# Kernel tuning notes

Hardware: AMD Instinct MI355X
Metric: run time of the kernel (lower is better)

Reference implementation:

```python
import jax, jax.numpy as jnp
import numpy as np

B, S, H, L = 4, 8192, 1024, 4
RATIOS = [1.0, 0.5, 0.25, 0.125]
H4 = H // 4


def _xavier(key, shape):
    fan_in, fan_out = shape[-2], shape[-1]
    std = np.sqrt(2.0 / (fan_in + fan_out)).astype(np.float32)
    return jax.random.normal(key, shape, dtype=jnp.float32) * std


def setup_inputs() -> dict:
    key = jax.random.key(0)
    ks = jax.random.split(key, 32)
    it = iter(ks)
    inp = {
        "keys": jax.random.normal(next(it), (B, S, H), dtype=jnp.float32),
        "values": jax.random.normal(next(it), (B, S, H), dtype=jnp.float32),
        # level predictors (same shape across levels -> stacked). Weights stored as [in, out].
        "Pw1": _xavier(next(it), (L, H, H4)),
        "Pb1": jnp.zeros((L, H4), dtype=jnp.float32),
        "Pw2": _xavier(next(it), (L, H4, 1)),
        "Pb2": jnp.zeros((L, 1), dtype=jnp.float32),
    }
    for l, r in enumerate(RATIOS):
        d = int(H * r)
        inp[f"cw1_{l}"] = _xavier(next(it), (H, d))
        inp[f"cb1_{l}"] = jnp.zeros((d,), dtype=jnp.float32)
        inp[f"cw2_{l}"] = _xavier(next(it), (d, H))
        inp[f"cb2_{l}"] = jnp.zeros((H,), dtype=jnp.float32)
    return inp


def reference(keys, values, Pw1, Pb1, Pw2, Pb2,
              cw1_0, cb1_0, cw2_0, cb2_0,
              cw1_1, cb1_1, cw2_1, cb2_1,
              cw1_2, cb1_2, cw2_2, cb2_2,
              cw1_3, cb1_3, cw2_3, cb2_3):
    comps = [
        (cw1_0, cb1_0, cw2_0, cb2_0),
        (cw1_1, cb1_1, cw2_1, cb2_1),
        (cw1_2, cb1_2, cw2_2, cb2_2),
        (cw1_3, cb1_3, cw2_3, cb2_3),
    ]

    def assign_levels(x):
        # per-level predictor: sigmoid(relu(x W1 + b1) W2 + b2) -> argmax over levels
        h = jax.nn.relu(jnp.einsum('bsh,lhd->lbsd', x, Pw1) + Pb1[:, None, None, :])
        p = jax.nn.sigmoid(jnp.einsum('lbsd,ldo->lbso', h, Pw2) + Pb2[:, None, None, :])
        return jnp.argmax(p[..., 0], axis=0)  # [B, S] int, first-max tiebreak like torch.argmax

    def compress(x, lev):
        out = jnp.zeros_like(x)
        for l, (w1, b1, w2, b2) in enumerate(comps):
            y = jax.nn.relu(x @ w1 + b1) @ w2 + b2  # bottleneck MLP for level l
            out = jnp.where((lev == l)[..., None], y, out)
        return out

    key_levels = assign_levels(keys)
    value_levels = assign_levels(values)
    return compress(keys, key_levels), compress(values, value_levels)
```

## Files before the change

### kernel.cpp

```cpp
#include <hip/hip_runtime.h>

#define NTOK 32768
#define MARGIN 0.08f

typedef __attribute__((ext_vector_type(8))) short bshort8;
typedef __attribute__((ext_vector_type(8))) unsigned short ushort8v;
typedef __attribute__((ext_vector_type(4))) float f32x4;

__device__ __forceinline__ unsigned short f2bf(float f) {
  unsigned u = __float_as_uint(f);
  u += 0x7fffu + ((u >> 16) & 1u);
  return (unsigned short)(u >> 16);
}
__device__ __forceinline__ float bf2f(unsigned short h) {
  return __uint_as_float((unsigned)h << 16);
}

__device__ __forceinline__ void gload16(const void* g, void* l) {
  __builtin_amdgcn_global_load_lds(
      (const __attribute__((address_space(1))) void*)g,
      (__attribute__((address_space(3))) void*)l, 16, 0, 0);
}

__global__ __launch_bounds__(256) void xconv_kernel(
    const float* __restrict__ keys, const float* __restrict__ vals,
    unsigned short* __restrict__ xbf) {
  const size_t stride = (size_t)gridDim.x * 256;
  const size_t half = (size_t)NTOK * 128;
  for (size_t u = (size_t)blockIdx.x * 256 + threadIdx.x;
       u < (size_t)2 * NTOK * 128; u += stride) {
    const float* s = (u < half) ? (keys + u * 8) : (vals + (u - half) * 8);
    float4 a = *(const float4*)s;
    float4 b = *(const float4*)(s + 4);
    ushort8v o;
    o[0] = f2bf(a.x); o[1] = f2bf(a.y); o[2] = f2bf(a.z); o[3] = f2bf(a.w);
    o[4] = f2bf(b.x); o[5] = f2bf(b.y); o[6] = f2bf(b.z); o[7] = f2bf(b.w);
    *(ushort8v*)(xbf + u * 8) = o;
  }
}

struct TrArgs {
  const float* src[12];
  unsigned short* dst[12];
  int R[12];
  int C[12];
};

__global__ __launch_bounds__(256) void convert_kernel(TrArgs ta) {
  __shared__ float t[32][33];
  const int mid = blockIdx.z;
  const int R = ta.R[mid], C = ta.C[mid];
  const int r0 = blockIdx.y * 32, c0 = blockIdx.x * 32;
  if (r0 >= R || c0 >= C) return;
  const float* __restrict__ src = ta.src[mid];
  unsigned short* __restrict__ dst = ta.dst[mid];
  const int tid = threadIdx.x;
#pragma unroll
  for (int it = 0; it < 4; ++it) {
    int r = it * 8 + (tid >> 5), c = tid & 31;
    t[r][c] = src[(size_t)(r0 + r) * C + c0 + c];
  }
  __syncthreads();
#pragma unroll
  for (int it = 0; it < 4; ++it) {
    int cc = it * 8 + (tid >> 5), rr = tid & 31;
    dst[(size_t)(c0 + cc) * R + r0 + rr] = f2bf(t[rr][cc]);
  }
}

#define M_PRED 0
#define M_L1   1
#define M_L2   2

struct GArgs {
  const unsigned short* xbf;
  const unsigned short* predW1T;
  const float* Pb1; const float* Pw2;
  float* logits;
  const unsigned short* cw1T[4];
  const unsigned short* cw2T[4];
  const float* cb1[4]; const float* cb2[4];
  unsigned short* h;
  const int* counts; const int* bins;
  const long long* hOff;
  float* out;
};

template<int MODE>
__global__ __launch_bounds__(256) void gemm_core(GArgs ga) {
  const int tid  = threadIdx.x;
  const int lane = tid & 63;
  const int wave = tid >> 6;

  int lev, tens, tile, n0;
  if constexpr (MODE == M_PRED) {
    const int combo = blockIdx.x;
    n0   = (combo & 1) * 128;
    lev  = (combo >> 1) & 3;
    tens = combo >> 3;
    tile = blockIdx.z;
  } else {
    n0   = blockIdx.x * 128;
    const int zz = blockIdx.y;
    lev  = zz & 3;
    tens = zz >> 2;
    tile = blockIdx.z;
  }
  const int z = tens * 4 + lev;
  const int d = 1024 >> lev;

  int cnt, K;
  const unsigned short* Bt;
  if constexpr (MODE == M_PRED) {
    cnt = NTOK; K = 1024;
    Bt = ga.predW1T + ((size_t)lev * 256 + n0) * 1024;
  } else if constexpr (MODE == M_L1) {
    cnt = ga.counts[z]; K = 1024;
    if (n0 >= d) return;
    Bt = ga.cw1T[lev] + (size_t)n0 * 1024;
  } else {
    cnt = ga.counts[z]; K = d;
    Bt = ga.cw2T[lev] + (size_t)n0 * (size_t)d;
  }
  if (tile * 128 >= cnt) return;
  const int nt = min(128, cnt - tile * 128);

  __shared__ __align__(16) char smem[33280];
  int* tokS = (int*)(smem + 32768);

  long long hoff = 0;
  if constexpr (MODE != M_PRED) hoff = ga.hOff[z];

  const int arow  = tid & 127;
  const int celem = (tid >> 7) * 8;
  const unsigned short* aP;
  if constexpr (MODE == M_PRED) {
    aP = ga.xbf + ((size_t)tens * NTOK + tile * 128 + arow) * 1024;
  } else if constexpr (MODE == M_L1) {
    int idx = tile * 128 + arow;
    if (idx >= cnt) idx = cnt - 1;
    aP = ga.xbf + ((size_t)tens * NTOK + ga.bins[(size_t)z * NTOK + idx]) * 1024;
  } else {
    int rg = tile * 128 + arow;
    if (rg >= cnt) rg = cnt - 1;
    aP = ga.h + hoff + (size_t)rg * d;
  }
  aP += celem;
  const unsigned short* bP = Bt + (size_t)arow * K + celem;

  if constexpr (MODE == M_L2) {
    if (tid < 128) {
      int idx = tile * 128 + tid;
      if (idx >= cnt) idx = cnt - 1;
      tokS[tid] = ga.bins[(size_t)z * NTOK + idx];
    }
  }

  f32x4 acc[4][4];
#pragma unroll
  for (int i = 0; i < 4; ++i)
#pragma unroll
    for (int j = 0; j < 4; ++j) acc[i][j] = (f32x4)0.f;

  const int wm = (wave & 1) * 64, wn = (wave >> 1) * 64;

  char* const As0 = smem + tid * 16;
  char* const As1 = As0 + 4096;
  char* const Bs0 = As0 + 16384;
  char* const Bs1 = As0 + 20480;

  gload16(aP,      As0); gload16(aP + 16, As1);
  gload16(bP,      Bs0); gload16(bP + 16, Bs1);
  aP += 32; bP += 32;
  __syncthreads();

  const int fro = (lane >> 4) * 2048 + (lane & 15) * 16;
  int bufo = 0;
  const int nk = K >> 5;
  for (int it = 0; it < nk; ++it) {
    if (it + 1 < nk) {
      const int bo = bufo ^ 8192;
      gload16(aP,      As0 + bo); gload16(aP + 16, As1 + bo);
      gload16(bP,      Bs0 + bo); gload16(bP + 16, Bs1 + bo);
      aP += 32; bP += 32;
    }
    const char* Ab = smem + bufo + fro;
    bshort8 af[4], bfr[4];
#pragma unroll
    for (int i = 0; i < 4; ++i)
      af[i] = *(const bshort8*)(Ab + (wm + i * 16) * 16);
#pragma unroll
    for (int j = 0; j < 4; ++j)
      bfr[j] = *(const bshort8*)(Ab + 16384 + (wn + j * 16) * 16);
#pragma unroll
    for (int i = 0; i < 4; ++i)
#pragma unroll
      for (int j = 0; j < 4; ++j)
        acc[i][j] = __builtin_amdgcn_mfma_f32_16x16x32_bf16(af[i], bfr[j], acc[i][j], 0, 0, 0);
    __syncthreads();
    bufo ^= 8192;
  }

  if constexpr (MODE == M_PRED) {
    const float* b1 = ga.Pb1 + lev * 256 + n0;
    const float* w2 = ga.Pw2 + lev * 256 + n0;
    float part[4][4];
#pragma unroll
    for (int i = 0; i < 4; ++i)
#pragma unroll
      for (int r = 0; r < 4; ++r) part[i][r] = 0.f;
#pragma unroll
    for (int j = 0; j < 4; ++j) {
      int col = wn + j * 16 + (lane & 15);
      float bb = b1[col], ww = w2[col];
#pragma unroll
      for (int i = 0; i < 4; ++i)
#pragma unroll
        for (int r = 0; r < 4; ++r)
          part[i][r] = fmaf(fmaxf(acc[i][j][r] + bb, 0.f), ww, part[i][r]);
    }
#pragma unroll
    for (int m = 1; m < 16; m <<= 1)
#pragma unroll
      for (int i = 0; i < 4; ++i)
#pragma unroll
        for (int r = 0; r < 4; ++r)
          part[i][r] += __shfl_xor(part[i][r], m, 64);
    if ((lane & 15) == 0) {
      float* lg = ga.logits + (size_t)z * NTOK;
#pragma unroll
      for (int i = 0; i < 4; ++i)
#pragma unroll
        for (int r = 0; r < 4; ++r) {
          int row = tile * 128 + wm + i * 16 + (lane >> 4) * 4 + r;
          atomicAdd(&lg[row], part[i][r]);
        }
    }
  } else if constexpr (MODE == M_L1) {
    const float* b1 = ga.cb1[lev];
    unsigned short* Hs = (unsigned short*)smem;
#pragma unroll
    for (int i = 0; i < 4; ++i)
#pragma unroll
      for (int j = 0; j < 4; ++j) {
        int col = wn + j * 16 + (lane & 15);
        float bb = b1[n0 + col];
#pragma unroll
        for (int r = 0; r < 4; ++r) {
          int row = wm + i * 16 + (lane >> 4) * 4 + r;
          Hs[row * 128 + col] = f2bf(fmaxf(acc[i][j][r] + bb, 0.f));
        }
      }
    __syncthreads();
    unsigned short* hout = ga.h + hoff;
#pragma unroll
    for (int p = 0; p < 8; ++p) {
      int idx = p * 256 + tid;
      int row = idx >> 4;
      int cc  = (idx & 15) * 8;
      int rg = tile * 128 + row;
      if (rg < cnt)
        *(uint4*)(hout + (size_t)rg * d + n0 + cc) = *(const uint4*)(Hs + row * 128 + cc);
    }
  } else {
    const float* b2 = ga.cb2[lev];
    float* outT = ga.out + (size_t)tens * NTOK * 1024;
#pragma unroll
    for (int i = 0; i < 4; ++i)
#pragma unroll
      for (int r = 0; r < 4; ++r) {
        int row = wm + i * 16 + (lane >> 4) * 4 + r;
        if (row < nt) {
          int tok = tokS[row];
#pragma unroll
          for (int j = 0; j < 4; ++j) {
            int col = n0 + wn + j * 16 + (lane & 15);
            outT[(size_t)tok * 1024 + col] = acc[i][j][r] + b2[col];
          }
        }
      }
  }
}

__global__ __launch_bounds__(256) void argmax_margin_kernel(
    const float* __restrict__ logits, const float* __restrict__ Pb2,
    int* __restrict__ counts, int* __restrict__ bins,
    int* __restrict__ rcnt, int* __restrict__ rlist) {
  int i = blockIdx.x * 256 + threadIdx.x;
  if (i >= 2 * NTOK) return;
  int tens = i >> 15;
  int tok  = i & (NTOK - 1);
  const float* lg = logits + (size_t)tens * 4 * NTOK;
  float best = lg[tok] + Pb2[0];
  int bl = 0;
  float sec = -3.4e38f;
#pragma unroll
  for (int l = 1; l < 4; ++l) {
    float v = lg[(size_t)l * NTOK + tok] + Pb2[l];
    if (v > best) { sec = best; best = v; bl = l; }
    else if (v > sec) sec = v;
  }
  if (best - sec < MARGIN) {
    int pos = atomicAdd(&rcnt[tens], 1);
    rlist[tens * NTOK + pos] = tok;
  } else {
    int bin = tens * 4 + bl;
    int pos = atomicAdd(&counts[bin], 1);
    bins[(size_t)bin * NTOK + pos] = tok;
  }
}

__global__ __launch_bounds__(256) void recheck_gemm(
    const float* __restrict__ keys, const float* __restrict__ vals,
    const float* __restrict__ Pw1, const float* __restrict__ Pb1,
    const float* __restrict__ Pw2, const float* __restrict__ Pb2,
    const int* __restrict__ rcnt, const int* __restrict__ rlist,
    float* __restrict__ logitsR) {
  const int tid  = threadIdx.x;
  const int lev  = blockIdx.y;
  const int tens = blockIdx.z;
  const int cnt  = rcnt[tens];
  const float* __restrict__ X = tens ? vals : keys;
  const float* __restrict__ W = Pw1 + (size_t)lev * 1024 * 256;

  __shared__ float Xs[32][68];
  __shared__ float Ws[32][256];
  __shared__ float red[64][33];
  __shared__ int tokS[64];

  const int tokg = tid >> 5;
  const int colg = tid & 31;

  for (int tile = blockIdx.x; tile * 64 < cnt; tile += gridDim.x) {
    __syncthreads();
    if (tid < 64) {
      int s = tile * 64 + tid;
      tokS[tid] = rlist[tens * NTOK + min(s, cnt - 1)];
    }
    __syncthreads();

    float acc[8][8];
#pragma unroll
    for (int t = 0; t < 8; ++t)
#pragma unroll
      for (int c = 0; c < 8; ++c) acc[t][c] = 0.f;

    for (int kc = 0; kc < 32; ++kc) {
      __syncthreads();
      {
        int j = tid;
        int t64 = j >> 3, kf4 = j & 7;
        float4 v = *(const float4*)&X[(size_t)tokS[t64] * 1024 + kc * 32 + kf4 * 4];
        Xs[kf4 * 4 + 0][t64] = v.x; Xs[kf4 * 4 + 1][t64] = v.y;
        Xs[kf4 * 4 + 2][t64] = v.z; Xs[kf4 * 4 + 3][t64] = v.w;
        j = tid + 256;
        t64 = j >> 3; kf4 = j & 7;
        float4 w = *(const float4*)&X[(size_t)tokS[t64] * 1024 + kc * 32 + kf4 * 4];
        Xs[kf4 * 4 + 0][t64] = w.x; Xs[kf4 * 4 + 1][t64] = w.y;
        Xs[kf4 * 4 + 2][t64] = w.z; Xs[kf4 * 4 + 3][t64] = w.w;
      }
#pragma unroll
      for (int s = 0; s < 8; ++s) {
        int j = tid + s * 256;
        int kr = j >> 6, cf4 = j & 63;
        *(float4*)&Ws[kr][cf4 * 4] =
            *(const float4*)&W[(size_t)(kc * 32 + kr) * 256 + cf4 * 4];
      }
      __syncthreads();
#pragma unroll 8
      for (int kk = 0; kk < 32; ++kk) {
        float4 xa = *(const float4*)&Xs[kk][tokg * 8];
        float4 xb = *(const float4*)&Xs[kk][tokg * 8 + 4];
        float4 wa = *(const float4*)&Ws[kk][colg * 8];
        float4 wb = *(const float4*)&Ws[kk][colg * 8 + 4];
        float xr[8] = {xa.x, xa.y, xa.z, xa.w, xb.x, xb.y, xb.z, xb.w};
        float wr[8] = {wa.x, wa.y, wa.z, wa.w, wb.x, wb.y, wb.z, wb.w};
#pragma unroll
        for (int t = 0; t < 8; ++t)
#pragma unroll
          for (int c = 0; c < 8; ++c)
            acc[t][c] = fmaf(xr[t], wr[c], acc[t][c]);
      }
    }

    const float* b1 = Pb1 + lev * 256;
    const float* w2 = Pw2 + lev * 256;
    float part[8];
#pragma unroll
    for (int t = 0; t < 8; ++t) part[t] = 0.f;
#pragma unroll
    for (int c = 0; c < 8; ++c) {
      float b1c = b1[colg * 8 + c];
      float w2c = w2[colg * 8 + c];
#pragma unroll
      for (int t = 0; t < 8; ++t)
        part[t] = fmaf(fmaxf(acc[t][c] + b1c, 0.f), w2c, part[t]);
    }
    __syncthreads();
#pragma unroll
    for (int t = 0; t < 8; ++t) red[tokg * 8 + t][colg] = part[t];
    __syncthreads();
    if (tid < 64 && tile * 64 + tid < cnt) {
      float s = Pb2[lev];
#pragma unroll
      for (int c = 0; c < 32; ++c) s += red[tid][c];
      logitsR[((size_t)tens * 4 + lev) * NTOK + tile * 64 + tid] = s;
    }
  }
}

__global__ __launch_bounds__(256) void recheck_argmax_kernel(
    const float* __restrict__ logitsR, const int* __restrict__ rcnt,
    const int* __restrict__ rlist, int* __restrict__ counts,
    int* __restrict__ bins) {
  int i = blockIdx.x * 256 + threadIdx.x;
  if (i >= 2 * NTOK) return;
  int tens = i >> 15;
  int slot = i & (NTOK - 1);
  if (slot >= rcnt[tens]) return;
  const float* lg = logitsR + (size_t)tens * 4 * NTOK;
  float best = lg[slot];
  int bl = 0;
#pragma unroll
  for (int l = 1; l < 4; ++l) {
    float v = lg[(size_t)l * NTOK + slot];
    if (v > best) { best = v; bl = l; }
  }
  int tok = rlist[tens * NTOK + slot];
  int bin = tens * 4 + bl;
  int pos = atomicAdd(&counts[bin], 1);
  bins[(size_t)bin * NTOK + pos] = tok;
}

__global__ void hoff_kernel(const int* __restrict__ counts,
                            long long* __restrict__ hOff) {
  long long off = 0;
  for (int b = 0; b < 8; ++b) {
    hOff[b] = off;
    off += (long long)counts[b] * (1024 >> (b & 3));
  }
}

extern "C" void kernel_launch(void* const* d_in, const int* in_sizes, int n_in,
                              void* d_out, int out_size, void* d_ws, size_t ws_size,
                              hipStream_t stream) {
  (void)in_sizes; (void)n_in; (void)out_size; (void)ws_size;
  const float* keys = (const float*)d_in[0];
  const float* vals = (const float*)d_in[1];
  const float* Pw1  = (const float*)d_in[2];
  const float* Pb1  = (const float*)d_in[3];
  const float* Pw2  = (const float*)d_in[4];
  const float* Pb2  = (const float*)d_in[5];

  char* base = (char*)d_ws;
  float* logits   = (float*)(base + 0);
  float* logitsR  = (float*)(base + 1048576);
  int*   bins     = (int*)(base + 2097152);
  int*   rlist    = (int*)(base + 3145728);
  int*   counts   = (int*)(base + 3407872);
  int*   rcnt     = (int*)(base + 3407872 + 32);
  long long* hOff = (long long*)(base + 3407936);
  unsigned short* predW1T = (unsigned short*)(base + 3408384);
  unsigned short* cw1T0 = (unsigned short*)(base + 5505536);
  unsigned short* cw1T1 = (unsigned short*)(base + 7602688);
  unsigned short* cw1T2 = (unsigned short*)(base + 8651264);
  unsigned short* cw1T3 = (unsigned short*)(base + 9175552);
  unsigned short* cw2T0 = (unsigned short*)(base + 9437696);
  unsigned short* cw2T1 = (unsigned short*)(base + 11534848);
  unsigned short* cw2T2 = (unsigned short*)(base + 12583424);
  unsigned short* cw2T3 = (unsigned short*)(base + 13107712);
  unsigned short* hpool = (unsigned short*)(base + 13369856);
  unsigned short* xbf   = (unsigned short*)(base + 147587584);

  hipMemsetAsync(logits, 0, 1048576, stream);
  hipMemsetAsync(counts, 0, 64, stream);

  xconv_kernel<<<dim3(2048), 256, 0, stream>>>(keys, vals, xbf);

  TrArgs ta;
  unsigned short* cw1T[4] = {cw1T0, cw1T1, cw1T2, cw1T3};
  unsigned short* cw2T[4] = {cw2T0, cw2T1, cw2T2, cw2T3};
  for (int l = 0; l < 4; ++l) {
    int d = 1024 >> l;
    ta.src[l] = Pw1 + (size_t)l * 1024 * 256;  ta.dst[l] = predW1T + (size_t)l * 256 * 1024;
    ta.R[l] = 1024; ta.C[l] = 256;
    ta.src[4 + l] = (const float*)d_in[6 + l * 4 + 0];  ta.dst[4 + l] = cw1T[l];
    ta.R[4 + l] = 1024; ta.C[4 + l] = d;
    ta.src[8 + l] = (const float*)d_in[6 + l * 4 + 2];  ta.dst[8 + l] = cw2T[l];
    ta.R[8 + l] = d; ta.C[8 + l] = 1024;
  }
  convert_kernel<<<dim3(32, 32, 12), 256, 0, stream>>>(ta);

  GArgs ga;
  ga.xbf = xbf;
  ga.predW1T = predW1T; ga.Pb1 = Pb1; ga.Pw2 = Pw2;
  ga.logits = logits;
  for (int l = 0; l < 4; ++l) {
    ga.cw1T[l] = cw1T[l];
    ga.cw2T[l] = cw2T[l];
    ga.cb1[l] = (const float*)d_in[6 + l * 4 + 1];
    ga.cb2[l] = (const float*)d_in[6 + l * 4 + 3];
  }
  ga.h = hpool; ga.counts = counts; ga.bins = bins; ga.hOff = hOff;
  ga.out = (float*)d_out;

  gemm_core<M_PRED><<<dim3(16, 1, 256), 256, 0, stream>>>(ga);
  argmax_margin_kernel<<<dim3(256), 256, 0, stream>>>(logits, Pb2, counts, bins, rcnt, rlist);
  recheck_gemm<<<dim3(32, 4, 2), 256, 0, stream>>>(keys, vals, Pw1, Pb1, Pw2, Pb2,
                                                   rcnt, rlist, logitsR);
  recheck_argmax_kernel<<<dim3(256), 256, 0, stream>>>(logitsR, rcnt, rlist, counts, bins);
  hoff_kernel<<<1, 1, 0, stream>>>(counts, hOff);
  gemm_core<M_L1><<<dim3(8, 8, 256), 256, 0, stream>>>(ga);
  gemm_core<M_L2><<<dim3(8, 8, 256), 256, 0, stream>>>(ga);
}
```

Before: 2.220 ms.

## Triple-buffer GEMM K-loop with vmcnt waits and raise recheck grid

Changes the shared GEMM core from double to triple buffering of the A/B tiles in LDS, using explicit s_waitcnt vmcnt and raw barriers so two k-steps of loads stay in flight. It also raises wave priority around the MFMA block and peels the last iteration. Separately, the recheck_gemm grid grows from 32 to 128 blocks in x to spread the recheck work over more CUs. The cost is more LDS per block (about 49KB), which may reduce occupancy, and the hand-written wait counts depend on the global_load_lds ordering being correct.

```diff
diff --git a/kernel.cpp b/kernel.cpp
--- a/kernel.cpp
+++ b/kernel.cpp
@@ -125,8 +125,8 @@
   if (tile * 128 >= cnt) return;
   const int nt = min(128, cnt - tile * 128);
 
-  __shared__ __align__(16) char smem[33280];
-  int* tokS = (int*)(smem + 32768);
+  __shared__ __align__(16) char smem[49664];
+  int* tokS = (int*)(smem + 49152);
 
   long long hoff = 0;
   if constexpr (MODE != M_PRED) hoff = ga.hOff[z];
@@ -164,24 +164,26 @@
 
   const int wm = (wave & 1) * 64, wn = (wave >> 1) * 64;
 
-  char* const As0 = smem + tid * 16;
-  char* const As1 = As0 + 4096;
-  char* const Bs0 = As0 + 16384;
-  char* const Bs1 = As0 + 20480;
-
-  gload16(aP,      As0); gload16(aP + 16, As1);
-  gload16(bP,      Bs0); gload16(bP + 16, Bs1);
+  char* const As = smem + tid * 16;
+
+  gload16(aP,      As);          gload16(aP + 16, As + 4096);
+  gload16(bP,      As + 8192);   gload16(bP + 16, As + 12288);
   aP += 32; bP += 32;
-  __syncthreads();
+  gload16(aP,      As + 16384);  gload16(aP + 16, As + 20480);
+  gload16(bP,      As + 24576);  gload16(bP + 16, As + 28672);
+  aP += 32; bP += 32;
 
   const int fro = (lane >> 4) * 2048 + (lane & 15) * 16;
+  const int nk = K >> 5;
   int bufo = 0;
-  const int nk = K >> 5;
-  for (int it = 0; it < nk; ++it) {
-    if (it + 1 < nk) {
-      const int bo = bufo ^ 8192;
-      gload16(aP,      As0 + bo); gload16(aP + 16, As1 + bo);
-      gload16(bP,      Bs0 + bo); gload16(bP + 16, Bs1 + bo);
+  int pfo  = 32768;
+
+  for (int it = 0; it < nk - 1; ++it) {
+    asm volatile("s_waitcnt vmcnt(4)" ::: "memory");
+    __builtin_amdgcn_s_barrier();
+    if (it + 2 < nk) {
+      gload16(aP,      As + pfo);         gload16(aP + 16, As + pfo + 4096);
+      gload16(bP,      As + pfo + 8192);  gload16(bP + 16, As + pfo + 12288);
       aP += 32; bP += 32;
     }
     const char* Ab = smem + bufo + fro;
@@ -191,15 +193,36 @@
       af[i] = *(const bshort8*)(Ab + (wm + i * 16) * 16);
 #pragma unroll
     for (int j = 0; j < 4; ++j)
-      bfr[j] = *(const bshort8*)(Ab + 16384 + (wn + j * 16) * 16);
+      bfr[j] = *(const bshort8*)(Ab + 8192 + (wn + j * 16) * 16);
+    __builtin_amdgcn_s_setprio(1);
 #pragma unroll
     for (int i = 0; i < 4; ++i)
 #pragma unroll
       for (int j = 0; j < 4; ++j)
         acc[i][j] = __builtin_amdgcn_mfma_f32_16x16x32_bf16(af[i], bfr[j], acc[i][j], 0, 0, 0);
-    __syncthreads();
-    bufo ^= 8192;
-  }
+    __builtin_amdgcn_s_setprio(0);
+    __builtin_amdgcn_sched_barrier(0);
+    bufo = (bufo == 32768) ? 0 : bufo + 16384;
+    pfo  = (pfo  == 32768) ? 0 : pfo  + 16384;
+  }
+  asm volatile("s_waitcnt vmcnt(0)" ::: "memory");
+  __builtin_amdgcn_s_barrier();
+  {
+    const char* Ab = smem + bufo + fro;
+    bshort8 af[4], bfr[4];
+#pragma unroll
+    for (int i = 0; i < 4; ++i)
+      af[i] = *(const bshort8*)(Ab + (wm + i * 16) * 16);
+#pragma unroll
+    for (int j = 0; j < 4; ++j)
+      bfr[j] = *(const bshort8*)(Ab + 8192 + (wn + j * 16) * 16);
+#pragma unroll
+    for (int i = 0; i < 4; ++i)
+#pragma unroll
+      for (int j = 0; j < 4; ++j)
+        acc[i][j] = __builtin_amdgcn_mfma_f32_16x16x32_bf16(af[i], bfr[j], acc[i][j], 0, 0, 0);
+  }
+  __syncthreads();
 
   if constexpr (MODE == M_PRED) {
     const float* b1 = ga.Pb1 + lev * 256 + n0;
@@ -506,8 +529,8 @@
 
   gemm_core<M_PRED><<<dim3(16, 1, 256), 256, 0, stream>>>(ga);
   argmax_margin_kernel<<<dim3(256), 256, 0, stream>>>(logits, Pb2, counts, bins, rcnt, rlist);
-  recheck_gemm<<<dim3(32, 4, 2), 256, 0, stream>>>(keys, vals, Pw1, Pb1, Pw2, Pb2,
-                                                   rcnt, rlist, logitsR);
+  recheck_gemm<<<dim3(128, 4, 2), 256, 0, stream>>>(keys, vals, Pw1, Pb1, Pw2, Pb2,
+                                                    rcnt, rlist, logitsR);
   recheck_argmax_kernel<<<dim3(256), 256, 0, stream>>>(logitsR, rcnt, rlist, counts, bins);
   hoff_kernel<<<1, 1, 0, stream>>>(counts, hOff);
   gemm_core<M_L1><<<dim3(8, 8, 256), 256, 0, stream>>>(ga);
```

After: 2.184 ms. About the same (-1.6%).
